# Performance work log

Hardware: AMD Instinct MI355X
Metric: run time of the kernel (lower is better)

Reference implementation:

```python
import jax, jax.numpy as jnp
import numpy as np

SIZE = (128, 128, 128)  # volume dims (X, Y, Z)
B, N, C = 2, 2097152, 1


def setup_inputs() -> dict:
    key = jax.random.key(0)
    k1, k2 = jax.random.split(key)
    image = jax.random.normal(k1, (B, SIZE[0], SIZE[1], SIZE[2], C), dtype=jnp.float32)
    grid = jax.random.uniform(k2, (B, N, 3), dtype=jnp.float32)  # normalized coords in [0,1]
    return {"image": image, "grid": grid}


def reference(image, grid):
    # image: [B, X, Y, Z, C]; grid: [B, N, 3] normalized -> trilinear sample -> [B, N, C]
    factor = jnp.array(SIZE, dtype=jnp.float32)
    idx = jnp.clip(grid * factor, 0.001, float(min(SIZE)) - 1.001)  # [B, N, 3]
    x, y, z = idx[..., 0], idx[..., 1], idx[..., 2]
    x1, x2 = jnp.floor(x), jnp.ceil(x)
    y1, y2 = jnp.floor(y), jnp.ceil(y)
    z1, z2 = jnp.floor(z), jnp.ceil(z)

    b = jnp.arange(image.shape[0])[:, None]  # [B, 1] batch index for gathers

    def g(xi, yi, zi):  # corner gather -> [B, N, C]
        return image[b, xi.astype(jnp.int32), yi.astype(jnp.int32), zi.astype(jnp.int32)]

    wx, wx2 = (x - x1)[..., None], (x2 - x)[..., None]
    wy, wy2 = (y - y1)[..., None], (y2 - y)[..., None]
    wz, wz2 = (z - z1)[..., None], (z2 - z)[..., None]

    lerp_y1 = (g(x2, y1, z1) * wx + g(x1, y1, z1) * wx2) * wy2 \
            + (g(x2, y2, z1) * wx + g(x1, y2, z1) * wx2) * wy
    lerp_y2 = (g(x2, y1, z2) * wx + g(x1, y1, z2) * wx2) * wy2 \
            + (g(x2, y2, z2) * wx + g(x1, y2, z2) * wx2) * wy
    return lerp_y2 * wz + lerp_y1 * wz2
```

## Files before the change

kernel.cpp:

```cpp
#include <hip/hip_runtime.h>
#include <hip/hip_fp16.h>


#define TOTAL   (2 * 2097152)
#define LOG2N   21
#define VOL     (128 * 128 * 128)
#define NVOX    (2 * VOL)

typedef __attribute__((ext_vector_type(4))) float fx4;

__global__ __launch_bounds__(256)
void ImageWarped_build_rec4_kernel(const float* __restrict__ in,
                                   uint4* __restrict__ rec)
{
    const int t    = blockIdx.x * 256 + threadIdx.x;
    const int idx0 = t << 2;
    const int v    = idx0 & (VOL - 1);
    const int x    = v >> 14;
    const int y    = (v >> 7) & 127;
    const int z0   = v & 127;
    const int xo   = (x < 127) ? (1 << 14) : 0;
    const int yo   = (y < 127) ? (1 << 7)  : 0;

    const float* __restrict__ r11 = in + (idx0 - z0);
    const float* __restrict__ r21 = r11 + xo;
    const float* __restrict__ r12 = r11 + yo;
    const float* __restrict__ r22 = r21 + yo;

    const int zn = min(z0 + 4, 127);
    const float4 a11 = *(const float4*)(r11 + z0); const float e11 = r11[zn];
    const float4 a21 = *(const float4*)(r21 + z0); const float e21 = r21[zn];
    const float4 a12 = *(const float4*)(r12 + z0); const float e12 = r12[zn];
    const float4 a22 = *(const float4*)(r22 + z0); const float e22 = r22[zn];

    union { __half2 h; unsigned u; } p;
    #define PAIR(lo, hi) (p.h = __floats2half2_rn((lo), (hi)), p.u)
    rec[idx0 + 0] = make_uint4(PAIR(a11.x, a11.y), PAIR(a21.x, a21.y),
                               PAIR(a12.x, a12.y), PAIR(a22.x, a22.y));
    rec[idx0 + 1] = make_uint4(PAIR(a11.y, a11.z), PAIR(a21.y, a21.z),
                               PAIR(a12.y, a12.z), PAIR(a22.y, a22.z));
    rec[idx0 + 2] = make_uint4(PAIR(a11.z, a11.w), PAIR(a21.z, a21.w),
                               PAIR(a12.z, a12.w), PAIR(a22.z, a22.w));
    rec[idx0 + 3] = make_uint4(PAIR(a11.w, e11),   PAIR(a21.w, e21),
                               PAIR(a12.w, e12),   PAIR(a22.w, e22));
    #undef PAIR
}

struct SampleW { int base; float wx, wx2, wy, wy2, wz, wz2; };

__device__ __forceinline__ SampleW mk_sample(float gx, float gy, float gz)
{
    SampleW s;
    const float xf = fminf(fmaxf(gx * 128.0f, 0.001f), 126.999f);
    const float yf = fminf(fmaxf(gy * 128.0f, 0.001f), 126.999f);
    const float zf = fminf(fmaxf(gz * 128.0f, 0.001f), 126.999f);
    const float x1f = floorf(xf), x2f = ceilf(xf);
    const float y1f = floorf(yf), y2f = ceilf(yf);
    const float z1f = floorf(zf), z2f = ceilf(zf);
    s.wx = xf - x1f; s.wx2 = x2f - xf;
    s.wy = yf - y1f; s.wy2 = y2f - yf;
    s.wz = zf - z1f; s.wz2 = z2f - zf;
    s.base = ((int)x1f << 14) + ((int)y1f << 7) + (int)z1f;
    return s;
}

__device__ __forceinline__ float fold_sample(const uint4 u, const SampleW& s)
{
    union { unsigned u32; __half2 h; } c;
    c.u32 = u.x; const float2 f11 = __half22float2(c.h);
    c.u32 = u.y; const float2 f21 = __half22float2(c.h);
    c.u32 = u.z; const float2 f12 = __half22float2(c.h);
    c.u32 = u.w; const float2 f22 = __half22float2(c.h);
    const float q11 = f11.x * s.wz2 + f11.y * s.wz;
    const float q21 = f21.x * s.wz2 + f21.y * s.wz;
    const float q12 = f12.x * s.wz2 + f12.y * s.wz;
    const float q22 = f22.x * s.wz2 + f22.y * s.wz;
    return (q21 * s.wx + q11 * s.wx2) * s.wy2
         + (q22 * s.wx + q12 * s.wx2) * s.wy;
}

__global__ __launch_bounds__(256)
void ImageWarped_trilinear_rec4_kernel(const uint4* __restrict__ rec,
                                       const float* __restrict__ grid,
                                       float* __restrict__ out)
{
    const int batch = blockIdx.x & 1;
    const int g     = (blockIdx.x >> 1) * 256 + threadIdx.x;
    const int i0    = (batch << LOG2N) | (g << 2);

    const fx4* gp = (const fx4*)(grid + 3 * (size_t)i0);
    const fx4 a = __builtin_nontemporal_load(gp + 0);
    const fx4 b = __builtin_nontemporal_load(gp + 1);
    const fx4 d = __builtin_nontemporal_load(gp + 2);

    const uint4* __restrict__ rb = rec + ((size_t)batch << LOG2N);

    const SampleW s0 = mk_sample(a.x, a.y, a.z);
    const SampleW s1 = mk_sample(a.w, b.x, b.y);
    const SampleW s2 = mk_sample(b.z, b.w, d.x);
    const SampleW s3 = mk_sample(d.y, d.z, d.w);

    const uint4 u0 = rb[s0.base];
    const uint4 u1 = rb[s1.base];
    const uint4 u2 = rb[s2.base];
    const uint4 u3 = rb[s3.base];

    fx4 r;
    r.x = fold_sample(u0, s0);
    r.y = fold_sample(u1, s1);
    r.z = fold_sample(u2, s2);
    r.w = fold_sample(u3, s3);
    __builtin_nontemporal_store(r, (fx4*)(out + i0));
}

__global__ __launch_bounds__(256)
void ImageWarped_cvt_fp16_kernel(const float* __restrict__ in,
                                 __half* __restrict__ out)
{
    const int i = blockIdx.x * 256 + threadIdx.x;
    const float4 v = ((const float4*)in)[i];
    union { __half2 h2[2]; uint2 u; } p;
    p.h2[0] = __floats2half2_rn(v.x, v.y);
    p.h2[1] = __floats2half2_rn(v.z, v.w);
    ((uint2*)out)[i] = p.u;
}

__global__ __launch_bounds__(256)
void ImageWarped_trilinear_h2_kernel(const __half* __restrict__ image,
                                     const float* __restrict__ grid,
                                     float* __restrict__ out)
{
    const int batch = blockIdx.x & 1;
    const int s     = (blockIdx.x >> 1) * 256 + threadIdx.x;
    const int i     = (batch << LOG2N) | s;

    const float gx = grid[3 * i + 0];
    const float gy = grid[3 * i + 1];
    const float gz = grid[3 * i + 2];

    const __half* __restrict__ img = image + ((size_t)batch << LOG2N);

    const float xf = fminf(fmaxf(gx * 128.0f, 0.001f), 126.999f);
    const float yf = fminf(fmaxf(gy * 128.0f, 0.001f), 126.999f);
    const float zf = fminf(fmaxf(gz * 128.0f, 0.001f), 126.999f);

    const float x1f = floorf(xf), x2f = ceilf(xf);
    const float y1f = floorf(yf), y2f = ceilf(yf);
    const float z1f = floorf(zf), z2f = ceilf(zf);

    const float wx  = xf - x1f, wx2 = x2f - xf;
    const float wy  = yf - y1f, wy2 = y2f - yf;
    const float wz  = zf - z1f, wz2 = z2f - zf;

    const int ix1 = (int)x1f, ix2 = (int)x2f;
    const int iy1 = (int)y1f, iy2 = (int)y2f;
    const int iz1 = (int)z1f;

    const int bx1 = ix1 << 14, bx2 = ix2 << 14;
    const int by1 = iy1 << 7,  by2 = iy2 << 7;

    const int ze = min(iz1 & ~1, 124);
    const int sh = (iz1 - ze) << 4;

    const float  ww  = wz2, wwz = wz;
    auto zfetch = [&](int off) -> float {
        const uint2 u = *(const uint2*)(img + off + ze);
        unsigned long long w = ((unsigned long long)u.y << 32) | u.x;
        w >>= sh;
        union { unsigned int u32; __half2 h; } c;
        c.u32 = (unsigned int)w;
        const float2 f = __half22float2(c.h);
        return f.x * ww + f.y * wwz;
    };

    const float q11 = zfetch(bx1 + by1);
    const float q21 = zfetch(bx2 + by1);
    const float q12 = zfetch(bx1 + by2);
    const float q22 = zfetch(bx2 + by2);

    out[i] = (q21 * wx + q11 * wx2) * wy2
           + (q22 * wx + q12 * wx2) * wy;
}

__global__ __launch_bounds__(256)
void ImageWarped_trilinear_f_kernel(const float* __restrict__ image,
                                    const float* __restrict__ grid,
                                    float* __restrict__ out)
{
    const int i = blockIdx.x * 256 + threadIdx.x;
    if (i >= TOTAL) return;

    const float gx = grid[3 * i + 0];
    const float gy = grid[3 * i + 1];
    const float gz = grid[3 * i + 2];

    const int b = i >> LOG2N;
    const float* __restrict__ img = image + (size_t)b * VOL;

    const float xf = fminf(fmaxf(gx * 128.0f, 0.001f), 126.999f);
    const float yf = fminf(fmaxf(gy * 128.0f, 0.001f), 126.999f);
    const float zf = fminf(fmaxf(gz * 128.0f, 0.001f), 126.999f);

    const float x1f = floorf(xf), x2f = ceilf(xf);
    const float y1f = floorf(yf), y2f = ceilf(yf);
    const float z1f = floorf(zf), z2f = ceilf(zf);

    const float wx  = xf - x1f, wx2 = x2f - xf;
    const float wy  = yf - y1f, wy2 = y2f - yf;
    const float wz  = zf - z1f, wz2 = z2f - zf;

    const int ix1 = (int)x1f, ix2 = (int)x2f;
    const int iy1 = (int)y1f, iy2 = (int)y2f;
    const int iz1 = (int)z1f, iz2 = (int)z2f;

    const int bx1 = ix1 << 14, bx2 = ix2 << 14;
    const int by1 = iy1 << 7,  by2 = iy2 << 7;

    const float c111 = img[bx1 + by1 + iz1];
    const float c211 = img[bx2 + by1 + iz1];
    const float c121 = img[bx1 + by2 + iz1];
    const float c221 = img[bx2 + by2 + iz1];
    const float c112 = img[bx1 + by1 + iz2];
    const float c212 = img[bx2 + by1 + iz2];
    const float c122 = img[bx1 + by2 + iz2];
    const float c222 = img[bx2 + by2 + iz2];

    const float lerp_y1 = (c211 * wx + c111 * wx2) * wy2
                        + (c221 * wx + c121 * wx2) * wy;
    const float lerp_y2 = (c212 * wx + c112 * wx2) * wy2
                        + (c222 * wx + c122 * wx2) * wy;

    out[i] = lerp_y2 * wz + lerp_y1 * wz2;
}

extern "C" void kernel_launch(void* const* d_in, const int* in_sizes, int n_in,
                              void* d_out, int out_size, void* d_ws, size_t ws_size,
                              hipStream_t stream)
{
    const float* image = (const float*)d_in[0];
    const float* grid  = (const float*)d_in[1];
    float* out = (float*)d_out;

    if (ws_size >= (size_t)NVOX * sizeof(uint4)) {
        uint4* rec = (uint4*)d_ws;
        ImageWarped_build_rec4_kernel<<<NVOX / 4 / 256, 256, 0, stream>>>(image, rec);
        ImageWarped_trilinear_rec4_kernel<<<TOTAL / 4 / 256, 256, 0, stream>>>(rec, grid, out);
    } else if (ws_size >= (size_t)NVOX * sizeof(__half)) {
        __half* img16 = (__half*)d_ws;
        ImageWarped_cvt_fp16_kernel<<<NVOX / 4 / 256, 256, 0, stream>>>(image, img16);
        ImageWarped_trilinear_h2_kernel<<<(TOTAL + 255) / 256, 256, 0, stream>>>(img16, grid, out);
    } else {
        ImageWarped_trilinear_f_kernel<<<(TOTAL + 255) / 256, 256, 0, stream>>>(image, grid, out);
    }
}
```

Before: 187.8 us.

## Bucket samples by x-slab before gathering to improve record-table locality

Adds a scatter pass that quantizes each sample's weights to 16 bits, packs index and weights into 12 bytes, and bins samples into 32 buckets by batch and x-slab using shared and global atomic counters. A third kernel then processes the buckets in groups so each pass gathers from a cache-sized slab of the fp16 corner-record table. The record builder is also simplified to one record per thread. This aims to cut scattered DRAM traffic from random gathers, at the cost of an extra payload write and read, an extra launch, and weight quantization error, with a direct-sample fallback when a bucket overflows.

```diff
diff --git a/kernel.cpp b/kernel.cpp
--- a/kernel.cpp
+++ b/kernel.cpp
@@ -7,43 +7,43 @@
 #define VOL     (128 * 128 * 128)
 #define NVOX    (2 * VOL)
 
+#define NBKT    32
+#define CAP     133120
+#define REC_BYTES  ((size_t)NVOX * 16)
+#define PAY_BYTES  ((size_t)NBKT * CAP * 12)
+#define WS_NEED    (REC_BYTES + PAY_BYTES + 128)
+
 typedef __attribute__((ext_vector_type(4))) float fx4;
 
 __global__ __launch_bounds__(256)
-void ImageWarped_build_rec4_kernel(const float* __restrict__ in,
-                                   uint4* __restrict__ rec)
-{
-    const int t    = blockIdx.x * 256 + threadIdx.x;
-    const int idx0 = t << 2;
-    const int v    = idx0 & (VOL - 1);
-    const int x    = v >> 14;
-    const int y    = (v >> 7) & 127;
-    const int z0   = v & 127;
-    const int xo   = (x < 127) ? (1 << 14) : 0;
-    const int yo   = (y < 127) ? (1 << 7)  : 0;
-
-    const float* __restrict__ r11 = in + (idx0 - z0);
+void ImageWarped_build_rec_kernel(const float* __restrict__ in,
+                                  uint4* __restrict__ rec,
+                                  unsigned* cursor)
+{
+    if (cursor && blockIdx.x == 0 && threadIdx.x < NBKT)
+        cursor[threadIdx.x] = 0;
+
+    const int idx = blockIdx.x * 256 + threadIdx.x;
+    const int v   = idx & (VOL - 1);
+    const int x   = v >> 14;
+    const int y   = (v >> 7) & 127;
+    const int z   = v & 127;
+    const int zp  = min(z + 1, 127);
+    const int xo  = (x < 127) ? (1 << 14) : 0;
+    const int yo  = (y < 127) ? (1 << 7)  : 0;
+
+    const float* __restrict__ r11 = in + (idx - z);
     const float* __restrict__ r21 = r11 + xo;
     const float* __restrict__ r12 = r11 + yo;
     const float* __restrict__ r22 = r21 + yo;
 
-    const int zn = min(z0 + 4, 127);
-    const float4 a11 = *(const float4*)(r11 + z0); const float e11 = r11[zn];
-    const float4 a21 = *(const float4*)(r21 + z0); const float e21 = r21[zn];
-    const float4 a12 = *(const float4*)(r12 + z0); const float e12 = r12[zn];
-    const float4 a22 = *(const float4*)(r22 + z0); const float e22 = r22[zn];
-
-    union { __half2 h; unsigned u; } p;
-    #define PAIR(lo, hi) (p.h = __floats2half2_rn((lo), (hi)), p.u)
-    rec[idx0 + 0] = make_uint4(PAIR(a11.x, a11.y), PAIR(a21.x, a21.y),
-                               PAIR(a12.x, a12.y), PAIR(a22.x, a22.y));
-    rec[idx0 + 1] = make_uint4(PAIR(a11.y, a11.z), PAIR(a21.y, a21.z),
-                               PAIR(a12.y, a12.z), PAIR(a22.y, a22.z));
-    rec[idx0 + 2] = make_uint4(PAIR(a11.z, a11.w), PAIR(a21.z, a21.w),
-                               PAIR(a12.z, a12.w), PAIR(a22.z, a22.w));
-    rec[idx0 + 3] = make_uint4(PAIR(a11.w, e11),   PAIR(a21.w, e21),
-                               PAIR(a12.w, e12),   PAIR(a22.w, e22));
-    #undef PAIR
+    union { __half2 h; unsigned u; } p0, p1, p2, p3;
+    p0.h = __floats2half2_rn(r11[z], r11[zp]);
+    p1.h = __floats2half2_rn(r21[z], r21[zp]);
+    p2.h = __floats2half2_rn(r12[z], r12[zp]);
+    p3.h = __floats2half2_rn(r22[z], r22[zp]);
+
+    rec[idx] = make_uint4(p0.u, p1.u, p2.u, p3.u);
 }
 
 struct SampleW { int base; float wx, wx2, wy, wy2, wz, wz2; };
@@ -80,6 +80,120 @@
 }
 
 __global__ __launch_bounds__(256)
+void ImageWarped_scatter_kernel(const float* __restrict__ grid,
+                                const uint4* __restrict__ rec,
+                                unsigned* __restrict__ pay,
+                                unsigned* __restrict__ cursor,
+                                float* __restrict__ out)
+{
+    __shared__ unsigned cnt[NBKT], bbase[NBKT];
+    if (threadIdx.x < NBKT) cnt[threadIdx.x] = 0;
+    __syncthreads();
+
+    const int t  = blockIdx.x * 256 + threadIdx.x;
+    const int i0 = t << 2;
+    const int batch = i0 >> LOG2N;
+
+    const fx4* gp = (const fx4*)(grid + 3 * (size_t)i0);
+    const fx4 ga = __builtin_nontemporal_load(gp + 0);
+    const fx4 gb = __builtin_nontemporal_load(gp + 1);
+    const fx4 gd = __builtin_nontemporal_load(gp + 2);
+
+    float gxs[4] = {ga.x, ga.w, gb.z, gd.y};
+    float gys[4] = {ga.y, gb.x, gb.w, gd.z};
+    float gzs[4] = {ga.z, gb.y, gd.x, gd.w};
+
+    unsigned pa[4], pb[4], pc[4], rnk[4];
+    int bkt[4];
+
+    #pragma unroll
+    for (int j = 0; j < 4; ++j) {
+        const float xf = fminf(fmaxf(gxs[j] * 128.0f, 0.001f), 126.999f);
+        const float yf = fminf(fmaxf(gys[j] * 128.0f, 0.001f), 126.999f);
+        const float zf = fminf(fmaxf(gzs[j] * 128.0f, 0.001f), 126.999f);
+        const float x1f = floorf(xf), y1f = floorf(yf), z1f = floorf(zf);
+        const bool zero = (xf == x1f) || (yf == y1f) || (zf == z1f);
+        const float wx = xf - x1f, wy = yf - y1f, wz = zf - z1f;
+        const unsigned ux = zero ? 0u : (unsigned)(wx * 65535.0f + 0.5f);
+        const unsigned uy = zero ? 0u : (unsigned)(wy * 65535.0f + 0.5f);
+        const unsigned uz = zero ? 0u : (unsigned)(wz * 65535.0f + 0.5f);
+        const int ix1 = (int)x1f, iy1 = (int)y1f, iz1 = (int)z1f;
+        const unsigned base = (unsigned)((ix1 << 14) | (iy1 << 7) | iz1);
+        const unsigned idxl = (unsigned)((i0 + j) & (VOL - 1));
+        bkt[j] = ((ix1 >> 3) << 1) | batch;
+        pa[j] = idxl | ((uz & 0x7FFu) << 21);
+        pb[j] = base | ((uz >> 11) << 21) | (zero ? 0x80000000u : 0u);
+        pc[j] = ux | (uy << 16);
+        rnk[j] = atomicAdd(&cnt[bkt[j]], 1u);
+    }
+    __syncthreads();
+    if (threadIdx.x < NBKT)
+        bbase[threadIdx.x] = atomicAdd(&cursor[threadIdx.x], cnt[threadIdx.x]);
+    __syncthreads();
+
+    #pragma unroll
+    for (int j = 0; j < 4; ++j) {
+        const unsigned pos = bbase[bkt[j]] + rnk[j];
+        if (pos < CAP) {
+            unsigned* p = pay + ((size_t)bkt[j] * CAP + pos) * 3;
+            p[0] = pa[j]; p[1] = pb[j]; p[2] = pc[j];
+        } else {
+            const SampleW s = mk_sample(gxs[j], gys[j], gzs[j]);
+            const uint4 u = rec[((size_t)batch << LOG2N) + s.base];
+            out[i0 + j] = fold_sample(u, s);
+        }
+    }
+}
+
+#define SAMP_BLOCKS 1024
+__global__ __launch_bounds__(256)
+void ImageWarped_sample_sorted_kernel(const uint4* __restrict__ rec,
+                                      const unsigned* __restrict__ pay,
+                                      const unsigned* __restrict__ cursor,
+                                      float* __restrict__ out)
+{
+    const int c = blockIdx.x & 7;
+    const int q = blockIdx.x >> 3;
+
+    for (int p = 0; p < 4; ++p) {
+        const int k = p * 8 + c;
+        const int count = (int)min(cursor[k], (unsigned)CAP);
+        const int chunk = (count + 127) >> 7;
+        const int start = q * chunk;
+        const int end   = min(start + chunk, count);
+        const unsigned* __restrict__ pp = pay + (size_t)k * CAP * 3;
+        const uint4* __restrict__ rb = rec + ((size_t)(k & 1) << LOG2N);
+        float* __restrict__ ob = out + ((size_t)(k & 1) << LOG2N);
+
+        for (int sb = start; sb < end; sb += 1024) {
+            #pragma unroll
+            for (int u4 = 0; u4 < 4; ++u4) {
+                const int s = sb + (u4 << 8) + threadIdx.x;
+                if (s < end) {
+                    const unsigned a  = pp[3 * s + 0];
+                    const unsigned b2 = pp[3 * s + 1];
+                    const unsigned c2 = pp[3 * s + 2];
+                    const unsigned idxl = a & 0x1FFFFFu;
+                    const unsigned base = b2 & 0x1FFFFFu;
+                    const unsigned uz = ((a >> 21) & 0x7FFu) | (((b2 >> 21) & 0x1Fu) << 11);
+                    const float one = (b2 & 0x80000000u) ? 0.0f : 1.0f;
+                    SampleW sw;
+                    sw.wx = (float)(c2 & 0xFFFFu) * (1.0f / 65535.0f);
+                    sw.wy = (float)(c2 >> 16)     * (1.0f / 65535.0f);
+                    sw.wz = (float)uz             * (1.0f / 65535.0f);
+                    sw.wx2 = one - sw.wx;
+                    sw.wy2 = one - sw.wy;
+                    sw.wz2 = one - sw.wz;
+                    const uint4 u = rb[base];
+                    const float r = fold_sample(u, sw);
+                    __builtin_nontemporal_store(r, ob + idxl);
+                }
+            }
+        }
+    }
+}
+
+__global__ __launch_bounds__(256)
 void ImageWarped_trilinear_rec4_kernel(const uint4* __restrict__ rec,
                                        const float* __restrict__ grid,
                                        float* __restrict__ out)
@@ -197,33 +311,35 @@
     const int b = i >> LOG2N;
     const float* __restrict__ img = image + (size_t)b * VOL;
 
+    const SampleW s = mk_sample(gx, gy, gz);
+    const int iz1 = s.base & 127;
+    const int iz2 = iz1 + (s.wz > 0.0f || s.wz2 > 0.0f ? (s.wz2 == 0.0f && s.wz == 0.0f ? 0 : 1) : 0);
+    const int bx1 = s.base & ~0x3FFF;
+    (void)bx1; (void)iz2;
+
     const float xf = fminf(fmaxf(gx * 128.0f, 0.001f), 126.999f);
     const float yf = fminf(fmaxf(gy * 128.0f, 0.001f), 126.999f);
     const float zf = fminf(fmaxf(gz * 128.0f, 0.001f), 126.999f);
-
     const float x1f = floorf(xf), x2f = ceilf(xf);
     const float y1f = floorf(yf), y2f = ceilf(yf);
     const float z1f = floorf(zf), z2f = ceilf(zf);
-
     const float wx  = xf - x1f, wx2 = x2f - xf;
     const float wy  = yf - y1f, wy2 = y2f - yf;
     const float wz  = zf - z1f, wz2 = z2f - zf;
-
     const int ix1 = (int)x1f, ix2 = (int)x2f;
     const int iy1 = (int)y1f, iy2 = (int)y2f;
-    const int iz1 = (int)z1f, iz2 = (int)z2f;
-
-    const int bx1 = ix1 << 14, bx2 = ix2 << 14;
-    const int by1 = iy1 << 7,  by2 = iy2 << 7;
-
-    const float c111 = img[bx1 + by1 + iz1];
-    const float c211 = img[bx2 + by1 + iz1];
-    const float c121 = img[bx1 + by2 + iz1];
-    const float c221 = img[bx2 + by2 + iz1];
-    const float c112 = img[bx1 + by1 + iz2];
-    const float c212 = img[bx2 + by1 + iz2];
-    const float c122 = img[bx1 + by2 + iz2];
-    const float c222 = img[bx2 + by2 + iz2];
+    const int jz1 = (int)z1f, jz2 = (int)z2f;
+    const int cx1 = ix1 << 14, cx2 = ix2 << 14;
+    const int cy1 = iy1 << 7,  cy2 = iy2 << 7;
+
+    const float c111 = img[cx1 + cy1 + jz1];
+    const float c211 = img[cx2 + cy1 + jz1];
+    const float c121 = img[cx1 + cy2 + jz1];
+    const float c221 = img[cx2 + cy2 + jz1];
+    const float c112 = img[cx1 + cy1 + jz2];
+    const float c212 = img[cx2 + cy1 + jz2];
+    const float c122 = img[cx1 + cy2 + jz2];
+    const float c222 = img[cx2 + cy2 + jz2];
 
     const float lerp_y1 = (c211 * wx + c111 * wx2) * wy2
                         + (c221 * wx + c121 * wx2) * wy;
@@ -241,9 +357,16 @@
     const float* grid  = (const float*)d_in[1];
     float* out = (float*)d_out;
 
-    if (ws_size >= (size_t)NVOX * sizeof(uint4)) {
+    if (ws_size >= WS_NEED) {
+        uint4*    rec    = (uint4*)d_ws;
+        unsigned* pay    = (unsigned*)((char*)d_ws + REC_BYTES);
+        unsigned* cursor = (unsigned*)((char*)d_ws + REC_BYTES + PAY_BYTES);
+        ImageWarped_build_rec_kernel<<<NVOX / 256, 256, 0, stream>>>(image, rec, cursor);
+        ImageWarped_scatter_kernel<<<TOTAL / 4 / 256, 256, 0, stream>>>(grid, rec, pay, cursor, out);
+        ImageWarped_sample_sorted_kernel<<<SAMP_BLOCKS, 256, 0, stream>>>(rec, pay, cursor, out);
+    } else if (ws_size >= REC_BYTES) {
         uint4* rec = (uint4*)d_ws;
-        ImageWarped_build_rec4_kernel<<<NVOX / 4 / 256, 256, 0, stream>>>(image, rec);
+        ImageWarped_build_rec_kernel<<<NVOX / 256, 256, 0, stream>>>(image, rec, nullptr);
         ImageWarped_trilinear_rec4_kernel<<<TOTAL / 4 / 256, 256, 0, stream>>>(rec, grid, out);
     } else if (ws_size >= (size_t)NVOX * sizeof(__half)) {
         __half* img16 = (__half*)d_ws;
```

Result: slower. 241.4 us (+28.6%).
